# Kernel tuning notes

Measured on AMD Instinct MI355X. Metric: run time of the kernel, lower is better.

## Reference

```python
import jax, jax.numpy as jnp
import numpy as np

EPS = 0.1        # entropic regularization (init kwarg eps)
MAX_ITER = 10    # init kwarg max_iter


def _M(C, u, v):
    # modified cost: (-C + u_i + v_j) / eps
    return (-C + u[:, None] + v[None, :]) / EPS


def setup_inputs() -> dict:
    key = jax.random.key(0)
    k1, k2 = jax.random.split(key)
    x = jax.random.normal(k1, (2048, 64), dtype=jnp.float32)
    y = jax.random.normal(k2, (2048, 64), dtype=jnp.float32)
    return {"x": x, "y": y}


def reference(x, y):
    n, m = x.shape[0], y.shape[0]
    # pairwise squared-L2 cost matrix [n, m] (p=2 with abs is just squared diff)
    C = jnp.sum(jnp.abs(x[:, None, :] - y[None, :, :]) ** 2, axis=-1)
    log_mu = jnp.log(jnp.full((n,), 1.0 / n, dtype=C.dtype) + 1e-8)
    log_nu = jnp.log(jnp.full((m,), 1.0 / m, dtype=C.dtype) + 1e-8)
    u0 = jnp.zeros((n,), C.dtype)
    v0 = jnp.zeros((m,), C.dtype)

    def step(carry, _):
        u, v, done = carry
        u_new = EPS * (log_mu - jax.nn.logsumexp(_M(C, u, v), axis=-1)) + u
        v_new = EPS * (log_nu - jax.nn.logsumexp(_M(C, u_new, v).T, axis=-1)) + v
        err = jnp.abs(u_new - u).sum()  # (u - u1).abs().sum(-1).mean() for 1D u
        # torch code breaks AFTER applying the update, so apply when not yet done
        u = jnp.where(done, u, u_new)
        v = jnp.where(done, v, v_new)
        done = done | (err < 0.1)
        return (u, v, done), None

    (u, v, _), _ = jax.lax.scan(step, (u0, v0, jnp.array(False)), None, length=MAX_ITER)
    pi = jnp.exp(_M(C, u, v))  # transport plan [n, m]
    cost = jnp.sum(pi * C)     # scalar Sinkhorn cost (batch_size = 1 case)
    return cost, pi, C
```

## Files before the change

kernel.cpp:

```cpp
#include <hip/hip_runtime.h>
#include <cmath>

#define NN 2048

#define EPSF 0.1f
#define K2 14.426950408889634f
#define LN2F 0.6931471805599453f

#define U_OFF   0
#define V_OFF   2048
#define ERR_OFF 4096
#define FLG_OFF 4112
#define DU_OFF  4128
#define CT_OFF  6176

__device__ __forceinline__ float fexp2(float x) { return __builtin_amdgcn_exp2f(x); }
__device__ __forceinline__ float flog2(float x) { return __builtin_amdgcn_logf(x); }

__global__ __launch_bounds__(256) void sink_cost(
        const float* __restrict__ x, const float* __restrict__ y,
        float* __restrict__ Cout, float* __restrict__ CT,
        float* __restrict__ wsz, float* __restrict__ cost) {
    __shared__ float xs[128][65];
    __shared__ float ys[64][65];
    int tid = threadIdx.x;
    int bj = blockIdx.x, bi = blockIdx.y;

    if (bi == 0 && bj == 0) {
        for (int k = tid; k < 6176; k += 256) wsz[k] = 0.f;
        if (tid == 0) cost[0] = 0.f;
    }

    const float4* x4 = (const float4*)x;
    const float4* y4 = (const float4*)y;
    for (int q = tid; q < 128 * 16; q += 256) {
        int r = q >> 4, dq = q & 15;
        float4 val = x4[(size_t)(bi * 128 + r) * 16 + dq];
        xs[r][dq * 4 + 0] = val.x; xs[r][dq * 4 + 1] = val.y;
        xs[r][dq * 4 + 2] = val.z; xs[r][dq * 4 + 3] = val.w;
    }
    for (int q = tid; q < 64 * 16; q += 256) {
        int r = q >> 4, dq = q & 15;
        float4 val = y4[(size_t)(bj * 64 + r) * 16 + dq];
        ys[r][dq * 4 + 0] = val.x; ys[r][dq * 4 + 1] = val.y;
        ys[r][dq * 4 + 2] = val.z; ys[r][dq * 4 + 3] = val.w;
    }
    __syncthreads();

    int tx = tid & 15, ty = tid >> 4;
    float acc[8][4];
#pragma unroll
    for (int ii = 0; ii < 8; ++ii)
#pragma unroll
        for (int jj = 0; jj < 4; ++jj) acc[ii][jj] = 0.f;

#pragma unroll 4
    for (int dd = 0; dd < 64; ++dd) {
        float xv[8], yv[4];
#pragma unroll
        for (int ii = 0; ii < 8; ++ii) xv[ii] = xs[ty + 16 * ii][dd];
#pragma unroll
        for (int jj = 0; jj < 4; ++jj) yv[jj] = ys[tx + 16 * jj][dd];
#pragma unroll
        for (int ii = 0; ii < 8; ++ii)
#pragma unroll
            for (int jj = 0; jj < 4; ++jj) {
                float d = xv[ii] - yv[jj];
                acc[ii][jj] = fmaf(d, d, acc[ii][jj]);
            }
    }

    __syncthreads();
#pragma unroll
    for (int ii = 0; ii < 8; ++ii)
#pragma unroll
        for (int jj = 0; jj < 4; ++jj) {
            int ri = ty + 16 * ii;
            int cj = tx + 16 * jj;
            Cout[(size_t)(bi * 128 + ri) * NN + bj * 64 + cj] = acc[ii][jj];
            xs[ri][cj] = acc[ii][jj];
        }
    __syncthreads();

    int c = tid >> 2, rb = (tid & 3) * 32;
    float4* dst = (float4*)(CT + (size_t)(bj * 64 + c) * NN + bi * 128 + rb);
#pragma unroll
    for (int k = 0; k < 8; ++k) {
        dst[k] = make_float4(xs[rb + 4 * k + 0][c], xs[rb + 4 * k + 1][c],
                             xs[rb + 4 * k + 2][c], xs[rb + 4 * k + 3][c]);
    }
}

__global__ __launch_bounds__(256, 2) void sink_u(
        const float* __restrict__ C, float* __restrict__ u,
        const float* __restrict__ v, float* __restrict__ du,
        const float* __restrict__ err, float* __restrict__ flag,
        int it, float log_mu) {
    int tid = threadIdx.x;
    if (it > 0) {
        if (flag[it - 1] != 0.f || err[it - 1] < 0.1f) {
            if (blockIdx.x == 0 && tid == 0) flag[it] = 1.f;
            return;
        }
    }
    int r0 = blockIdx.x * 4;
    int w = tid >> 6, l = tid & 63;

    float4 va = *(const float4*)(v + 4 * tid);
    float4 vb = *(const float4*)(v + 1024 + 4 * tid);
    float vK[8] = { va.x * K2, va.y * K2, va.z * K2, va.w * K2,
                    vb.x * K2, vb.y * K2, vb.z * K2, vb.w * K2 };

    float a[4][8];
#pragma unroll
    for (int r = 0; r < 4; ++r) {
        const float* row = C + (size_t)(r0 + r) * NN + 4 * tid;
        a[r][0] = fmaf(-K2, row[0], vK[0]);
        a[r][1] = fmaf(-K2, row[1], vK[1]);
        a[r][2] = fmaf(-K2, row[2], vK[2]);
        a[r][3] = fmaf(-K2, row[3], vK[3]);
        a[r][4] = fmaf(-K2, row[1024], vK[4]);
        a[r][5] = fmaf(-K2, row[1025], vK[5]);
        a[r][6] = fmaf(-K2, row[1026], vK[6]);
        a[r][7] = fmaf(-K2, row[1027], vK[7]);
    }

    float m4[4];
#pragma unroll
    for (int r = 0; r < 4; ++r) {
        float q0 = fmaxf(fmaxf(a[r][0], a[r][1]), fmaxf(a[r][2], a[r][3]));
        float q1 = fmaxf(fmaxf(a[r][4], a[r][5]), fmaxf(a[r][6], a[r][7]));
        m4[r] = fmaxf(q0, q1);
    }
#pragma unroll
    for (int off = 1; off < 64; off <<= 1)
#pragma unroll
        for (int r = 0; r < 4; ++r)
            m4[r] = fmaxf(m4[r], __shfl_xor(m4[r], off));
    __shared__ float wsm[4][4], wss[4][4];
    if (l == 0)
#pragma unroll
        for (int r = 0; r < 4; ++r) wsm[w][r] = m4[r];
    __syncthreads();
    float M4[4];
#pragma unroll
    for (int r = 0; r < 4; ++r)
        M4[r] = fmaxf(fmaxf(wsm[0][r], wsm[1][r]), fmaxf(wsm[2][r], wsm[3][r]));

    float s4[4];
#pragma unroll
    for (int r = 0; r < 4; ++r) {
        float t0 = fexp2(a[r][0] - M4[r]) + fexp2(a[r][1] - M4[r]);
        float t1 = fexp2(a[r][2] - M4[r]) + fexp2(a[r][3] - M4[r]);
        float t2 = fexp2(a[r][4] - M4[r]) + fexp2(a[r][5] - M4[r]);
        float t3 = fexp2(a[r][6] - M4[r]) + fexp2(a[r][7] - M4[r]);
        s4[r] = (t0 + t1) + (t2 + t3);
    }
#pragma unroll
    for (int off = 1; off < 64; off <<= 1)
#pragma unroll
        for (int r = 0; r < 4; ++r)
            s4[r] += __shfl_xor(s4[r], off);
    if (l == 0)
#pragma unroll
        for (int r = 0; r < 4; ++r) wss[w][r] = s4[r];
    __syncthreads();
    if (tid < 4) {
        float S = (wss[0][tid] + wss[1][tid]) + (wss[2][tid] + wss[3][tid]);
        float un = EPSF * (log_mu - LN2F * (M4[tid] + flog2(S)));
        du[r0 + tid] = fabsf(un - u[r0 + tid]);
        u[r0 + tid] = un;
    }
    if (blockIdx.x == 0 && tid == 0) flag[it] = 0.f;
}

__global__ __launch_bounds__(256, 2) void sink_v(
        const float* __restrict__ CT, float* __restrict__ v,
        const float* __restrict__ u, const float* __restrict__ du,
        float* __restrict__ err, const float* __restrict__ flag,
        int it, float log_nu) {
    if (flag[it] != 0.f) return;
    int tid = threadIdx.x;
    int j0 = blockIdx.x * 4;
    int w = tid >> 6, l = tid & 63;

    float4 ua = *(const float4*)(u + 4 * tid);
    float4 ub = *(const float4*)(u + 1024 + 4 * tid);
    float uK[8] = { ua.x * K2, ua.y * K2, ua.z * K2, ua.w * K2,
                    ub.x * K2, ub.y * K2, ub.z * K2, ub.w * K2 };

    float a[4][8];
#pragma unroll
    for (int r = 0; r < 4; ++r) {
        const float* row = CT + (size_t)(j0 + r) * NN;
        float4 c0 = *(const float4*)(row + 4 * tid);
        float4 c1 = *(const float4*)(row + 1024 + 4 * tid);
        a[r][0] = fmaf(-K2, c0.x, uK[0]);
        a[r][1] = fmaf(-K2, c0.y, uK[1]);
        a[r][2] = fmaf(-K2, c0.z, uK[2]);
        a[r][3] = fmaf(-K2, c0.w, uK[3]);
        a[r][4] = fmaf(-K2, c1.x, uK[4]);
        a[r][5] = fmaf(-K2, c1.y, uK[5]);
        a[r][6] = fmaf(-K2, c1.z, uK[6]);
        a[r][7] = fmaf(-K2, c1.w, uK[7]);
    }

    float m4[4];
#pragma unroll
    for (int r = 0; r < 4; ++r) {
        float q0 = fmaxf(fmaxf(a[r][0], a[r][1]), fmaxf(a[r][2], a[r][3]));
        float q1 = fmaxf(fmaxf(a[r][4], a[r][5]), fmaxf(a[r][6], a[r][7]));
        m4[r] = fmaxf(q0, q1);
    }
#pragma unroll
    for (int off = 1; off < 64; off <<= 1)
#pragma unroll
        for (int r = 0; r < 4; ++r)
            m4[r] = fmaxf(m4[r], __shfl_xor(m4[r], off));
    __shared__ float wsm[4][4], wss[4][4];
    if (l == 0)
#pragma unroll
        for (int r = 0; r < 4; ++r) wsm[w][r] = m4[r];
    __syncthreads();
    float M4[4];
#pragma unroll
    for (int r = 0; r < 4; ++r)
        M4[r] = fmaxf(fmaxf(wsm[0][r], wsm[1][r]), fmaxf(wsm[2][r], wsm[3][r]));

    float s4[4];
#pragma unroll
    for (int r = 0; r < 4; ++r) {
        float t0 = fexp2(a[r][0] - M4[r]) + fexp2(a[r][1] - M4[r]);
        float t1 = fexp2(a[r][2] - M4[r]) + fexp2(a[r][3] - M4[r]);
        float t2 = fexp2(a[r][4] - M4[r]) + fexp2(a[r][5] - M4[r]);
        float t3 = fexp2(a[r][6] - M4[r]) + fexp2(a[r][7] - M4[r]);
        s4[r] = (t0 + t1) + (t2 + t3);
    }
#pragma unroll
    for (int off = 1; off < 64; off <<= 1)
#pragma unroll
        for (int r = 0; r < 4; ++r)
            s4[r] += __shfl_xor(s4[r], off);
    if (l == 0)
#pragma unroll
        for (int r = 0; r < 4; ++r) wss[w][r] = s4[r];
    __syncthreads();
    if (tid < 4) {
        float S = (wss[0][tid] + wss[1][tid]) + (wss[2][tid] + wss[3][tid]);
        v[j0 + tid] = EPSF * (log_nu - LN2F * (M4[tid] + flog2(S)));
    }

    if (blockIdx.x == 0) {
        float t = 0.f;
#pragma unroll
        for (int k = 0; k < 8; ++k) t += du[tid + 256 * k];
#pragma unroll
        for (int off = 1; off < 64; off <<= 1) t += __shfl_xor(t, off);
        __shared__ float sl[4];
        if (l == 0) sl[w] = t;
        __syncthreads();
        if (tid == 0) err[it] = (sl[0] + sl[1]) + (sl[2] + sl[3]);
    }
}

__global__ __launch_bounds__(256, 2) void sink_pi(
        const float* __restrict__ C, const float* __restrict__ u,
        const float* __restrict__ v, float* __restrict__ pi,
        float* __restrict__ cost) {
    int tid = threadIdx.x;
    const float4* v4 = (const float4*)v;
    float local = 0.f;
    for (int rr = 0; rr < 4; ++rr) {
        int i = blockIdx.x * 4 + rr;
        float ui = u[i];
        const float* row = C + (size_t)i * NN;
        float* prow = pi + (size_t)i * NN;
        for (int k = tid; k < NN / 4; k += 256) {
            float c0 = row[4 * k + 0], c1 = row[4 * k + 1];
            float c2 = row[4 * k + 2], c3 = row[4 * k + 3];
            float4 vv = v4[k];
            float p0 = fexp2((ui + vv.x - c0) * K2);
            float p1 = fexp2((ui + vv.y - c1) * K2);
            float p2 = fexp2((ui + vv.z - c2) * K2);
            float p3 = fexp2((ui + vv.w - c3) * K2);
            prow[4 * k + 0] = p0;
            prow[4 * k + 1] = p1;
            prow[4 * k + 2] = p2;
            prow[4 * k + 3] = p3;
            local = fmaf(p0, c0, local);
            local = fmaf(p1, c1, local);
            local = fmaf(p2, c2, local);
            local = fmaf(p3, c3, local);
        }
    }
#pragma unroll
    for (int off = 1; off < 64; off <<= 1) local += __shfl_xor(local, off);
    __shared__ float sl[4];
    if ((tid & 63) == 0) sl[tid >> 6] = local;
    __syncthreads();
    if (tid == 0) atomicAdd(cost, sl[0] + sl[1] + sl[2] + sl[3]);
}

extern "C" void kernel_launch(void* const* d_in, const int* in_sizes, int n_in,
                              void* d_out, int out_size, void* d_ws, size_t ws_size,
                              hipStream_t stream) {
    const float* x = (const float*)d_in[0];
    const float* y = (const float*)d_in[1];
    float* out  = (float*)d_out;
    float* cost = out;
    float* pi   = out + 1;
    float* Cout = out + 1 + (size_t)NN * NN;

    float* ws   = (float*)d_ws;
    float* u    = ws + U_OFF;
    float* v    = ws + V_OFF;
    float* err  = ws + ERR_OFF;
    float* flag = ws + FLG_OFF;
    float* du   = ws + DU_OFF;
    float* CT   = ws + CT_OFF;

    float log_mu = (float)log(1.0 / 2048.0 + 1e-8);

    sink_cost<<<dim3(32, 16), 256, 0, stream>>>(x, y, Cout, CT, ws, cost);
    for (int it = 0; it < 10; ++it) {
        sink_u<<<512, 256, 0, stream>>>(Cout, u, v, du, err, flag, it, log_mu);
        sink_v<<<512, 256, 0, stream>>>(CT, v, u, du, err, flag, it, log_mu);
    }
    sink_pi<<<512, 256, 0, stream>>>(Cout, u, v, pi, cost);
}
```

Before: 131.1 us.

## Use norm expansion for cost matrix and halve rows per Sinkhorn block

The cost kernel now computes squared distances as |x|^2 + |y|^2 - 2x·y, with per-row norms precomputed in shared memory, so the inner loop is a single FMA per pair instead of a subtract plus an FMA. The u and v update kernels each handle two rows per block instead of four, launch twice as many blocks and raise the occupancy hint, to spread the memory-bound log-sum-exp passes over more of the GPU. The expansion can lose precision through cancellation when x and y are close, and smaller blocks add launch and reduction overhead per row.

```diff
diff --git a/kernel.cpp b/kernel.cpp
--- a/kernel.cpp
+++ b/kernel.cpp
@@ -23,6 +23,7 @@
         float* __restrict__ wsz, float* __restrict__ cost) {
     __shared__ float xs[128][65];
     __shared__ float ys[64][65];
+    __shared__ float xn[128], yn[64];
     int tid = threadIdx.x;
     int bj = blockIdx.x, bi = blockIdx.y;
 
@@ -47,6 +48,20 @@
     }
     __syncthreads();
 
+    if (tid < 128) {
+        float s = 0.f;
+#pragma unroll 8
+        for (int d = 0; d < 64; ++d) s = fmaf(xs[tid][d], xs[tid][d], s);
+        xn[tid] = s;
+    } else if (tid < 192) {
+        int r = tid - 128;
+        float s = 0.f;
+#pragma unroll 8
+        for (int d = 0; d < 64; ++d) s = fmaf(ys[r][d], ys[r][d], s);
+        yn[r] = s;
+    }
+    __syncthreads();
+
     int tx = tid & 15, ty = tid >> 4;
     float acc[8][4];
 #pragma unroll
@@ -64,12 +79,15 @@
 #pragma unroll
         for (int ii = 0; ii < 8; ++ii)
 #pragma unroll
-            for (int jj = 0; jj < 4; ++jj) {
-                float d = xv[ii] - yv[jj];
-                acc[ii][jj] = fmaf(d, d, acc[ii][jj]);
-            }
-    }
-
+            for (int jj = 0; jj < 4; ++jj)
+                acc[ii][jj] = fmaf(xv[ii], yv[jj], acc[ii][jj]);
+    }
+
+    float xnr[8], ynr[4];
+#pragma unroll
+    for (int ii = 0; ii < 8; ++ii) xnr[ii] = xn[ty + 16 * ii];
+#pragma unroll
+    for (int jj = 0; jj < 4; ++jj) ynr[jj] = yn[tx + 16 * jj];
     __syncthreads();
 #pragma unroll
     for (int ii = 0; ii < 8; ++ii)
@@ -77,8 +95,9 @@
         for (int jj = 0; jj < 4; ++jj) {
             int ri = ty + 16 * ii;
             int cj = tx + 16 * jj;
-            Cout[(size_t)(bi * 128 + ri) * NN + bj * 64 + cj] = acc[ii][jj];
-            xs[ri][cj] = acc[ii][jj];
+            float c = fmaf(-2.f, acc[ii][jj], xnr[ii] + ynr[jj]);
+            Cout[(size_t)(bi * 128 + ri) * NN + bj * 64 + cj] = c;
+            xs[ri][cj] = c;
         }
     __syncthreads();
 
@@ -91,7 +110,7 @@
     }
 }
 
-__global__ __launch_bounds__(256, 2) void sink_u(
+__global__ __launch_bounds__(256, 4) void sink_u(
         const float* __restrict__ C, float* __restrict__ u,
         const float* __restrict__ v, float* __restrict__ du,
         const float* __restrict__ err, float* __restrict__ flag,
@@ -103,7 +122,7 @@
             return;
         }
     }
-    int r0 = blockIdx.x * 4;
+    int r0 = blockIdx.x * 2;
     int w = tid >> 6, l = tid & 63;
 
     float4 va = *(const float4*)(v + 4 * tid);
@@ -111,9 +130,9 @@
     float vK[8] = { va.x * K2, va.y * K2, va.z * K2, va.w * K2,
                     vb.x * K2, vb.y * K2, vb.z * K2, vb.w * K2 };
 
-    float a[4][8];
-#pragma unroll
-    for (int r = 0; r < 4; ++r) {
+    float a[2][8];
+#pragma unroll
+    for (int r = 0; r < 2; ++r) {
         const float* row = C + (size_t)(r0 + r) * NN + 4 * tid;
         a[r][0] = fmaf(-K2, row[0], vK[0]);
         a[r][1] = fmaf(-K2, row[1], vK[1]);
@@ -125,63 +144,63 @@
         a[r][7] = fmaf(-K2, row[1027], vK[7]);
     }
 
-    float m4[4];
-#pragma unroll
-    for (int r = 0; r < 4; ++r) {
+    float m2[2];
+#pragma unroll
+    for (int r = 0; r < 2; ++r) {
         float q0 = fmaxf(fmaxf(a[r][0], a[r][1]), fmaxf(a[r][2], a[r][3]));
         float q1 = fmaxf(fmaxf(a[r][4], a[r][5]), fmaxf(a[r][6], a[r][7]));
-        m4[r] = fmaxf(q0, q1);
+        m2[r] = fmaxf(q0, q1);
     }
 #pragma unroll
     for (int off = 1; off < 64; off <<= 1)
 #pragma unroll
-        for (int r = 0; r < 4; ++r)
-            m4[r] = fmaxf(m4[r], __shfl_xor(m4[r], off));
-    __shared__ float wsm[4][4], wss[4][4];
+        for (int r = 0; r < 2; ++r)
+            m2[r] = fmaxf(m2[r], __shfl_xor(m2[r], off));
+    __shared__ float wsm[4][2], wss[4][2];
     if (l == 0)
 #pragma unroll
-        for (int r = 0; r < 4; ++r) wsm[w][r] = m4[r];
-    __syncthreads();
-    float M4[4];
-#pragma unroll
-    for (int r = 0; r < 4; ++r)
-        M4[r] = fmaxf(fmaxf(wsm[0][r], wsm[1][r]), fmaxf(wsm[2][r], wsm[3][r]));
-
-    float s4[4];
-#pragma unroll
-    for (int r = 0; r < 4; ++r) {
-        float t0 = fexp2(a[r][0] - M4[r]) + fexp2(a[r][1] - M4[r]);
-        float t1 = fexp2(a[r][2] - M4[r]) + fexp2(a[r][3] - M4[r]);
-        float t2 = fexp2(a[r][4] - M4[r]) + fexp2(a[r][5] - M4[r]);
-        float t3 = fexp2(a[r][6] - M4[r]) + fexp2(a[r][7] - M4[r]);
-        s4[r] = (t0 + t1) + (t2 + t3);
+        for (int r = 0; r < 2; ++r) wsm[w][r] = m2[r];
+    __syncthreads();
+    float M2[2];
+#pragma unroll
+    for (int r = 0; r < 2; ++r)
+        M2[r] = fmaxf(fmaxf(wsm[0][r], wsm[1][r]), fmaxf(wsm[2][r], wsm[3][r]));
+
+    float s2[2];
+#pragma unroll
+    for (int r = 0; r < 2; ++r) {
+        float t0 = fexp2(a[r][0] - M2[r]) + fexp2(a[r][1] - M2[r]);
+        float t1 = fexp2(a[r][2] - M2[r]) + fexp2(a[r][3] - M2[r]);
+        float t2 = fexp2(a[r][4] - M2[r]) + fexp2(a[r][5] - M2[r]);
+        float t3 = fexp2(a[r][6] - M2[r]) + fexp2(a[r][7] - M2[r]);
+        s2[r] = (t0 + t1) + (t2 + t3);
     }
 #pragma unroll
     for (int off = 1; off < 64; off <<= 1)
 #pragma unroll
-        for (int r = 0; r < 4; ++r)
-            s4[r] += __shfl_xor(s4[r], off);
+        for (int r = 0; r < 2; ++r)
+            s2[r] += __shfl_xor(s2[r], off);
     if (l == 0)
 #pragma unroll
-        for (int r = 0; r < 4; ++r) wss[w][r] = s4[r];
-    __syncthreads();
-    if (tid < 4) {
+        for (int r = 0; r < 2; ++r) wss[w][r] = s2[r];
+    __syncthreads();
+    if (tid < 2) {
         float S = (wss[0][tid] + wss[1][tid]) + (wss[2][tid] + wss[3][tid]);
-        float un = EPSF * (log_mu - LN2F * (M4[tid] + flog2(S)));
+        float un = EPSF * (log_mu - LN2F * (M2[tid] + flog2(S)));
         du[r0 + tid] = fabsf(un - u[r0 + tid]);
         u[r0 + tid] = un;
     }
     if (blockIdx.x == 0 && tid == 0) flag[it] = 0.f;
 }
 
-__global__ __launch_bounds__(256, 2) void sink_v(
+__global__ __launch_bounds__(256, 4) void sink_v(
         const float* __restrict__ CT, float* __restrict__ v,
         const float* __restrict__ u, const float* __restrict__ du,
         float* __restrict__ err, const float* __restrict__ flag,
         int it, float log_nu) {
     if (flag[it] != 0.f) return;
     int tid = threadIdx.x;
-    int j0 = blockIdx.x * 4;
+    int j0 = blockIdx.x * 2;
     int w = tid >> 6, l = tid & 63;
 
     float4 ua = *(const float4*)(u + 4 * tid);
@@ -189,9 +208,9 @@
     float uK[8] = { ua.x * K2, ua.y * K2, ua.z * K2, ua.w * K2,
                     ub.x * K2, ub.y * K2, ub.z * K2, ub.w * K2 };
 
-    float a[4][8];
-#pragma unroll
-    for (int r = 0; r < 4; ++r) {
+    float a[2][8];
+#pragma unroll
+    for (int r = 0; r < 2; ++r) {
         const float* row = CT + (size_t)(j0 + r) * NN;
         float4 c0 = *(const float4*)(row + 4 * tid);
         float4 c1 = *(const float4*)(row + 1024 + 4 * tid);
@@ -205,49 +224,49 @@
         a[r][7] = fmaf(-K2, c1.w, uK[7]);
     }
 
-    float m4[4];
-#pragma unroll
-    for (int r = 0; r < 4; ++r) {
+    float m2[2];
+#pragma unroll
+    for (int r = 0; r < 2; ++r) {
         float q0 = fmaxf(fmaxf(a[r][0], a[r][1]), fmaxf(a[r][2], a[r][3]));
         float q1 = fmaxf(fmaxf(a[r][4], a[r][5]), fmaxf(a[r][6], a[r][7]));
-        m4[r] = fmaxf(q0, q1);
+        m2[r] = fmaxf(q0, q1);
     }
 #pragma unroll
     for (int off = 1; off < 64; off <<= 1)
 #pragma unroll
-        for (int r = 0; r < 4; ++r)
-            m4[r] = fmaxf(m4[r], __shfl_xor(m4[r], off));
-    __shared__ float wsm[4][4], wss[4][4];
+        for (int r = 0; r < 2; ++r)
+            m2[r] = fmaxf(m2[r], __shfl_xor(m2[r], off));
+    __shared__ float wsm[4][2], wss[4][2];
     if (l == 0)
 #pragma unroll
-        for (int r = 0; r < 4; ++r) wsm[w][r] = m4[r];
-    __syncthreads();
-    float M4[4];
-#pragma unroll
-    for (int r = 0; r < 4; ++r)
-        M4[r] = fmaxf(fmaxf(wsm[0][r], wsm[1][r]), fmaxf(wsm[2][r], wsm[3][r]));
-
-    float s4[4];
-#pragma unroll
-    for (int r = 0; r < 4; ++r) {
-        float t0 = fexp2(a[r][0] - M4[r]) + fexp2(a[r][1] - M4[r]);
-        float t1 = fexp2(a[r][2] - M4[r]) + fexp2(a[r][3] - M4[r]);
-        float t2 = fexp2(a[r][4] - M4[r]) + fexp2(a[r][5] - M4[r]);
-        float t3 = fexp2(a[r][6] - M4[r]) + fexp2(a[r][7] - M4[r]);
-        s4[r] = (t0 + t1) + (t2 + t3);
+        for (int r = 0; r < 2; ++r) wsm[w][r] = m2[r];
+    __syncthreads();
+    float M2[2];
+#pragma unroll
+    for (int r = 0; r < 2; ++r)
+        M2[r] = fmaxf(fmaxf(wsm[0][r], wsm[1][r]), fmaxf(wsm[2][r], wsm[3][r]));
+
+    float s2[2];
+#pragma unroll
+    for (int r = 0; r < 2; ++r) {
+        float t0 = fexp2(a[r][0] - M2[r]) + fexp2(a[r][1] - M2[r]);
+        float t1 = fexp2(a[r][2] - M2[r]) + fexp2(a[r][3] - M2[r]);
+        float t2 = fexp2(a[r][4] - M2[r]) + fexp2(a[r][5] - M2[r]);
+        float t3 = fexp2(a[r][6] - M2[r]) + fexp2(a[r][7] - M2[r]);
+        s2[r] = (t0 + t1) + (t2 + t3);
     }
 #pragma unroll
     for (int off = 1; off < 64; off <<= 1)
 #pragma unroll
-        for (int r = 0; r < 4; ++r)
-            s4[r] += __shfl_xor(s4[r], off);
+        for (int r = 0; r < 2; ++r)
+            s2[r] += __shfl_xor(s2[r], off);
     if (l == 0)
 #pragma unroll
-        for (int r = 0; r < 4; ++r) wss[w][r] = s4[r];
-    __syncthreads();
-    if (tid < 4) {
+        for (int r = 0; r < 2; ++r) wss[w][r] = s2[r];
+    __syncthreads();
+    if (tid < 2) {
         float S = (wss[0][tid] + wss[1][tid]) + (wss[2][tid] + wss[3][tid]);
-        v[j0 + tid] = EPSF * (log_nu - LN2F * (M4[tid] + flog2(S)));
+        v[j0 + tid] = EPSF * (log_nu - LN2F * (M2[tid] + flog2(S)));
     }
 
     if (blockIdx.x == 0) {
@@ -323,8 +342,8 @@
 
     sink_cost<<<dim3(32, 16), 256, 0, stream>>>(x, y, Cout, CT, ws, cost);
     for (int it = 0; it < 10; ++it) {
-        sink_u<<<512, 256, 0, stream>>>(Cout, u, v, du, err, flag, it, log_mu);
-        sink_v<<<512, 256, 0, stream>>>(CT, v, u, du, err, flag, it, log_mu);
+        sink_u<<<1024, 256, 0, stream>>>(Cout, u, v, du, err, flag, it, log_mu);
+        sink_v<<<1024, 256, 0, stream>>>(CT, v, u, du, err, flag, it, log_mu);
     }
     sink_pi<<<512, 256, 0, stream>>>(Cout, u, v, pi, cost);
 }
```

Result: faster. 126.3 us (-3.7%).
